# Kernel tuning notes

Hardware: AMD Instinct MI355X
Metric: run time of the kernel (lower is better)

Reference implementation:

```python
import jax, jax.numpy as jnp
import numpy as np

D_MODEL = 1024
H = 16
D_K = D_MODEL // H
D_FF = 4096
EPS = 1e-6
NEG = -1e9


def setup_inputs() -> dict:
    key = jax.random.key(0)
    ks = jax.random.split(key, 8)
    B, S = 2, 2048
    src = jax.random.normal(ks[0], (B, S, D_MODEL), dtype=jnp.float32)
    src_mask = jnp.ones((B, 1, 1, S), dtype=jnp.int32)
    sc = 1.0 / np.sqrt(D_MODEL)
    wq = jax.random.normal(ks[1], (D_MODEL, D_MODEL), jnp.float32) * sc
    wk = jax.random.normal(ks[2], (D_MODEL, D_MODEL), jnp.float32) * sc
    wv = jax.random.normal(ks[3], (D_MODEL, D_MODEL), jnp.float32) * sc
    wo = jax.random.normal(ks[4], (D_MODEL, D_MODEL), jnp.float32) * sc
    w1 = jax.random.normal(ks[5], (D_FF, D_MODEL), jnp.float32) * sc
    b1 = jnp.zeros((D_FF,), jnp.float32)
    w2 = jax.random.normal(ks[6], (D_MODEL, D_FF), jnp.float32) * (1.0 / np.sqrt(D_FF))
    b2 = jnp.zeros((D_MODEL,), jnp.float32)
    a1 = jnp.ones((1,), jnp.float32)
    be1 = jnp.zeros((1,), jnp.float32)
    a2 = jnp.ones((1,), jnp.float32)
    be2 = jnp.zeros((1,), jnp.float32)
    return dict(src=src, src_mask=src_mask, wq=wq, wk=wk, wv=wv, wo=wo,
                w1=w1, b1=b1, w2=w2, b2=b2, a1=a1, be1=be1, a2=a2, be2=be2)


def layer_norm(x, alpha, bias):
    # torch: mean + unbiased std (ddof=1), eps added to std
    mean = jnp.mean(x, axis=-1, keepdims=True)
    std = jnp.sqrt(jnp.var(x, axis=-1, keepdims=True, ddof=1))
    return alpha * (x - mean) / (std + EPS) + bias


def mha(x, mask, wq, wk, wv, wo):
    B, S, _ = x.shape
    def split(t):  # [B,S,D] -> [B,H,S,D_K]
        return t.reshape(B, S, H, D_K).transpose(0, 2, 1, 3)
    q = split(x @ wq.T)
    k = split(x @ wk.T)
    v = split(x @ wv.T)
    scores = jnp.einsum('bhqd,bhkd->bhqk', q, k) / np.sqrt(D_K)
    scores = jnp.where(mask == 0, NEG, scores)
    attn = jax.nn.softmax(scores, axis=-1)
    out = jnp.einsum('bhqk,bhkd->bhqd', attn, v)
    out = out.transpose(0, 2, 1, 3).reshape(B, S, D_MODEL)
    return out @ wo.T


def reference(src, src_mask, wq, wk, wv, wo, w1, b1, w2, b2, a1, be1, a2, be2):
    x = layer_norm(src, a1, be1)
    src = src + mha(x, src_mask, wq, wk, wv, wo)
    x = layer_norm(src, a2, be2)
    ff = jax.nn.relu(x @ w1.T + b1) @ w2.T + b2
    return src + ff
```

## Files before the change

kernel.cpp:

```cpp
#include <hip/hip_runtime.h>
#include <hip/hip_bf16.h>

typedef unsigned short u16;
typedef unsigned int u32;
typedef float floatx4 __attribute__((ext_vector_type(4)));
typedef __bf16 bf16x8 __attribute__((ext_vector_type(8)));
typedef u16 ushort4v __attribute__((ext_vector_type(4)));
typedef u16 ushort8v __attribute__((ext_vector_type(8)));

#define DEVI static __device__ __forceinline__

DEVI u16 f2bf(float f) {
    u32 u = __builtin_bit_cast(u32, f);
    u += 0x7fffu + ((u >> 16) & 1u);
    return (u16)(u >> 16);
}
DEVI float bf2f(u16 h) { return __builtin_bit_cast(float, (u32)h << 16); }

DEVI float fexp2(float x) { return __builtin_amdgcn_exp2f(x); }

DEVI u32 cvtpk_bf16(float lo, float hi) {
    u32 r;
    asm("v_cvt_pk_bf16_f32 %0, %1, %2" : "=v"(r) : "v"(lo), "v"(hi));
    return r;
}

DEVI void async_cp16(const u16* g, u16* l) {
    __builtin_amdgcn_global_load_lds((const __attribute__((address_space(1))) u32*)g,
                                     (__attribute__((address_space(3))) u32*)l, 16, 0, 0);
}

template<int N> DEVI void wait_vmcnt() {
    if constexpr (N == 0)      asm volatile("s_waitcnt vmcnt(0)" ::: "memory");
    else if constexpr (N == 2) asm volatile("s_waitcnt vmcnt(2)" ::: "memory");
    else if constexpr (N == 3) asm volatile("s_waitcnt vmcnt(3)" ::: "memory");
    else if constexpr (N == 4) asm volatile("s_waitcnt vmcnt(4)" ::: "memory");
    else if constexpr (N == 6) asm volatile("s_waitcnt vmcnt(6)" ::: "memory");
    else static_assert(N == 0, "add vmcnt case");
}

#define PH_BAR() asm volatile("s_barrier" ::: "memory")

template<bool QKV3, int NSPLIT, bool BIAS, bool RELU, bool VTW>
__global__ __launch_bounds__(512, 2) void gemm8p(
    const u16* __restrict__ A,
    const u16* __restrict__ W0, const u16* __restrict__ W1, const u16* __restrict__ W2,
    const float* __restrict__ bias,
    void* __restrict__ o0, void* __restrict__ o1, void* __restrict__ o2,
    void* __restrict__ o3, int K, int lda, int Nper, int NX)
{
    __shared__ __align__(16) u16 As[2][2][8192];
    __shared__ __align__(16) u16 Bs[2][2][8192];
    const int tid = threadIdx.x;
    const int w = tid >> 6, lane = tid & 63;
    const int q = lane >> 4, ml = lane & 15;
    const int wr = w >> 2, wc = w & 3;
    int bx = blockIdx.x, by = blockIdx.y;
    {
        const int gx = gridDim.x, gy = gridDim.y;
        int L = by * gx + bx;
        int xcd = L & 7, s = L >> 3;
        int mb = gy >> 3;
        by = xcd * mb + s % mb;
        bx = s / mb;
    }
    const int m0 = by * 256;
    size_t kbase = 0;
    const u16* W = W0;
    void* outp = o0;
    if (NSPLIT > 1) {
        int part = bx / NX; bx -= part * NX; kbase = (size_t)part * K;
        outp = (part == 0) ? o0 : (part == 1 ? o1 : (part == 2 ? o2 : o3));
    }
    int n0 = bx * 256;
    bool vwrite = false;
    if (QKV3) {
        int sel = n0 / Nper; n0 -= sel * Nper;
        W = (sel == 0) ? W0 : (sel == 1 ? W1 : W2);
        outp = (sel == 0) ? o0 : (sel == 1 ? o1 : o2);
        if (VTW) vwrite = (sel == 2);
    }

    auto stA = [&](int d, int kh, int kt) {
#pragma unroll
        for (int p = 0; p < 2; ++p) {
            int c = p * 512 + tid;
            int r = c >> 2;
            int sc = (c & 3) ^ ((r >> 1) & 3);
            async_cp16(A + (size_t)(m0 + r) * lda + kbase + kt + kh * 32 + sc * 8,
                       &As[d][kh][(p * 512 + w * 64) * 8]);
        }
    };
    auto stB = [&](int d, int kh, int kt) {
#pragma unroll
        for (int p = 0; p < 2; ++p) {
            int c = p * 512 + tid;
            int r = c >> 2;
            int sc = (c & 3) ^ ((r >> 1) & 3);
            async_cp16(W + (size_t)(n0 + r) * lda + kbase + kt + kh * 32 + sc * 8,
                       &Bs[d][kh][(p * 512 + w * 64) * 8]);
        }
    };
    auto rdA = [&](int d, int kh, int i) -> bf16x8 {
        int rm = wr * 128 + i * 16 + ml;
        return *(const bf16x8*)&As[d][kh][(rm * 4 + (q ^ ((rm >> 1) & 3))) * 8];
    };
    auto rdB = [&](int d, int kh, int j) -> bf16x8 {
        int rn = wc * 64 + j * 16 + ml;
        return *(const bf16x8*)&Bs[d][kh][(rn * 4 + (q ^ ((rn >> 1) & 3))) * 8];
    };

    const floatx4 fzero = {0.f, 0.f, 0.f, 0.f};
    floatx4 acc[8][4];
#pragma unroll
    for (int i = 0; i < 8; ++i)
#pragma unroll
        for (int j = 0; j < 4; ++j) acc[i][j] = fzero;

#define PHASE(d, kh, ih, STG, VM)                                              \
    {                                                                          \
        if (ih == 0) {                                                         \
            _Pragma("unroll")                                                  \
            for (int j = 0; j < 4; ++j) bfr[j] = rdB(d, kh, j);                \
        }                                                                      \
        _Pragma("unroll")                                                      \
        for (int ii = 0; ii < 4; ++ii) af[ii] = rdA(d, kh, (ih) * 4 + ii);     \
        STG;                                                                   \
        if (VM) wait_vmcnt<4>();                                               \
        PH_BAR();                                                              \
        __builtin_amdgcn_s_setprio(1);                                         \
        _Pragma("unroll")                                                      \
        for (int ii = 0; ii < 4; ++ii)                                         \
            _Pragma("unroll")                                                  \
            for (int j = 0; j < 4; ++j)                                        \
                acc[(ih) * 4 + ii][j] = __builtin_amdgcn_mfma_f32_16x16x32_bf16( \
                    af[ii], bfr[j], acc[(ih) * 4 + ii][j], 0, 0, 0);           \
        __builtin_amdgcn_s_setprio(0);                                         \
        PH_BAR();                                                              \
    }

    const int R = K >> 7;
    stA(0, 0, 0); stB(0, 0, 0); stA(0, 1, 0); stB(0, 1, 0);
    wait_vmcnt<0>();
    PH_BAR();

    for (int rr = 0; rr < R; ++rr) {
        const int kt1 = rr * 128 + 64;
        const int kt2 = (rr * 128 + 128 <= K - 64) ? rr * 128 + 128
                                                   : K - 64;
        bf16x8 af[4], bfr[4];
        PHASE(0, 0, 0, stA(1, 0, kt1), 0)
        PHASE(0, 0, 1, stB(1, 0, kt1), 1)
        PHASE(0, 1, 0, stA(1, 1, kt1), 0)
        PHASE(0, 1, 1, stB(1, 1, kt1), 1)
        PHASE(1, 0, 0, stA(0, 0, kt2), 0)
        PHASE(1, 0, 1, stB(0, 0, kt2), 1)
        PHASE(1, 1, 0, stA(0, 1, kt2), 0)
        PHASE(1, 1, 1, stB(0, 1, kt2), 1)
    }
#undef PHASE
    wait_vmcnt<0>();

#pragma unroll
    for (int j = 0; j < 4; ++j) {
        int gn = n0 + wc * 64 + j * 16 + ml;
        float bj = 0.f;
        if (BIAS) bj = bias[gn];
#pragma unroll
        for (int i = 0; i < 8; ++i) {
            int gm0 = m0 + wr * 128 + i * 16 + q * 4;
            if (VTW && vwrite) {
                int bb = gm0 >> 11, sres = gm0 & 2047;
                ushort4v o = {f2bf(acc[i][j][0]), f2bf(acc[i][j][1]),
                              f2bf(acc[i][j][2]), f2bf(acc[i][j][3])};
                *(ushort4v*)&((u16*)o3)[(size_t)(bb * 1024 + gn) * 2048 + sres] = o;
            } else {
#pragma unroll
                for (int r = 0; r < 4; ++r) {
                    size_t idx = (size_t)(gm0 + r) * Nper + gn;
                    float v = acc[i][j][r] + bj;
                    if (RELU) v = fmaxf(v, 0.f);
                    ((u16*)outp)[idx] = f2bf(v);
                }
            }
        }
    }
}

template<int BM, int BN, int RW, int CW, bool BIAS, bool RELU, bool RESID, bool OBF16>
__global__ __launch_bounds__(256) void gemm_nt(
    const u16* __restrict__ A, const u16* __restrict__ W0,
    const float* __restrict__ bias, const float* __restrict__ resid,
    void* __restrict__ o0, int K, int lda, int Nper)
{
    static_assert(RW * CW == 4, "4 waves");
    constexpr int WM = BM / RW, WN = BN / CW;
    constexpr int MI = WM / 16, NI = WN / 16;
    constexpr int LPT = BM / 64 + BN / 64;
    __shared__ __align__(16) u16 As[3][BM * 32];
    __shared__ __align__(16) u16 Bs[3][BN * 32];
    const int tid = threadIdx.x;
    const int w = tid >> 6, lane = tid & 63;
    const int q = lane >> 4, ml = lane & 15;
    const int wr = w / CW, wc = w % CW;
    int bx = blockIdx.x, by = blockIdx.y;
    {
        const int gx = gridDim.x, gy = gridDim.y;
        int L = by * gx + bx;
        int xcd = L & 7, s = L >> 3;
        int mb = gy >> 3;
        by = xcd * mb + s % mb;
        bx = s / mb;
    }
    const int m0 = by * BM;
    const u16* W = W0;
    int n0 = bx * BN;

    auto stage = [&](int buf, int kt) {
#pragma unroll
        for (int p = 0; p < BM / 64; ++p) {
            int g = p * 256 + tid;
            int r = g >> 2, s = g & 3;
            int c = s ^ ((r >> 1) & 3);
            async_cp16(A + (size_t)(m0 + r) * lda + kt + c * 8,
                       &As[buf][(p * 256 + w * 64) * 8]);
        }
#pragma unroll
        for (int p = 0; p < BN / 64; ++p) {
            int g = p * 256 + tid;
            int r = g >> 2, s = g & 3;
            int c = s ^ ((r >> 1) & 3);
            async_cp16(W + (size_t)(n0 + r) * lda + kt + c * 8,
                       &Bs[buf][(p * 256 + w * 64) * 8]);
        }
    };

    const floatx4 fzero = {0.f, 0.f, 0.f, 0.f};
    floatx4 acc[MI][NI];
#pragma unroll
    for (int i = 0; i < MI; ++i)
#pragma unroll
        for (int j = 0; j < NI; ++j) acc[i][j] = fzero;

    const int nt = K >> 5;
    stage(0, 0);
    stage(1, 32);
    int cb = 0, nb = 2;
    for (int it = 0, kt = 0; it < nt; ++it, kt += 32) {
        wait_vmcnt<LPT>();
        __builtin_amdgcn_s_barrier();
        __builtin_amdgcn_sched_barrier(0);
        if (it + 2 < nt) stage(nb, kt + 64);
        __builtin_amdgcn_sched_barrier(0);
        const u16* Asb = As[cb];
        const u16* Bsb = Bs[cb];
        bf16x8 af[MI], bfr[NI];
#pragma unroll
        for (int i = 0; i < MI; ++i) {
            int rm = wr * WM + i * 16 + ml;
            int s = q ^ ((rm >> 1) & 3);
            af[i] = *(const bf16x8*)&Asb[(rm * 4 + s) * 8];
        }
#pragma unroll
        for (int j = 0; j < NI; ++j) {
            int rn = wc * WN + j * 16 + ml;
            int s = q ^ ((rn >> 1) & 3);
            bfr[j] = *(const bf16x8*)&Bsb[(rn * 4 + s) * 8];
        }
#pragma unroll
        for (int i = 0; i < MI; ++i)
#pragma unroll
            for (int j = 0; j < NI; ++j)
                acc[i][j] = __builtin_amdgcn_mfma_f32_16x16x32_bf16(af[i], bfr[j], acc[i][j], 0, 0, 0);
        cb = cb == 2 ? 0 : cb + 1;
        nb = nb == 2 ? 0 : nb + 1;
    }

#pragma unroll
    for (int j = 0; j < NI; ++j) {
        int gn = n0 + wc * WN + j * 16 + ml;
        float bj = 0.f;
        if (BIAS) bj = bias[gn];
#pragma unroll
        for (int i = 0; i < MI; ++i) {
            int gm0 = m0 + wr * WM + i * 16 + q * 4;
#pragma unroll
            for (int r = 0; r < 4; ++r) {
                size_t idx = (size_t)(gm0 + r) * Nper + gn;
                float v = acc[i][j][r] + bj;
                if (RELU) v = fmaxf(v, 0.f);
                if (RESID) v += resid[idx];
                if (OBF16) ((u16*)o0)[idx] = f2bf(v);
                else       ((float*)o0)[idx] = v;
            }
        }
    }
}

__global__ __launch_bounds__(256, 2) void flash9(
    const u16* __restrict__ Q, const u16* __restrict__ Kg,
    const u16* __restrict__ Vt, const float* __restrict__ biasv,
    u16* __restrict__ O)
{
    __shared__ __align__(16) u16 smem[24576];
    const int tid = threadIdx.x;
    const int w = tid >> 6, lane = tid & 63;
    const int qw = w & 1, kv = w >> 1;
    const int q = lane >> 4, ml = lane & 15;
    const int b = blockIdx.y >> 4, h = blockIdx.y & 15;
    const size_t rowQ = (size_t)(b * 2048 + blockIdx.x * 128);
    const float KSC = 0.125f * 1.4426950408889634f;
    const floatx4 fzero = {0.f, 0.f, 0.f, 0.f};

    bf16x8 qa[4][2];
#pragma unroll
    for (int qg = 0; qg < 4; ++qg)
#pragma unroll
        for (int c = 0; c < 2; ++c)
            qa[qg][c] = *(const bf16x8*)&Q[(rowQ + qw * 64 + qg * 16 + ml) * 1024
                                           + h * 64 + q * 8 + c * 32];

    auto stage = [&](int buf, int it) {
        {
            int row = tid >> 3, sl = tid & 7;
            int ch = sl ^ ((row & 3) | (((row >> 3) & 1) << 2));
#pragma unroll
            for (int hf = 0; hf < 2; ++hf)
                async_cp16(Kg + (size_t)(b * 2048 + hf * 1024 + it * 32 + row) * 1024
                               + h * 64 + ch * 8,
                           &smem[(hf * 3 + buf) * 2048 + w * 512]);
        }
        {
            int row = tid >> 2, sl = tid & 3;
            int ch = sl ^ ((row >> 1) & 3);
#pragma unroll
            for (int hf = 0; hf < 2; ++hf)
                async_cp16(Vt + (size_t)(b * 1024 + h * 64 + row) * 2048
                               + hf * 1024 + it * 32 + ch * 8,
                           &smem[12288 + (hf * 3 + buf) * 2048 + w * 512]);
        }
    };

    floatx4 oacc[4][4];
    float lsum[4] = {0.f, 0.f, 0.f, 0.f};
#pragma unroll
    for (int qg = 0; qg < 4; ++qg)
#pragma unroll
        for (int d = 0; d < 4; ++d) oacc[qg][d] = fzero;

    const int swk = (ml & 3) | (((ml >> 2) & 1) << 2);
    const int re = ((ml >> 2) << 3) + (ml & 3);

    stage(0, 0);
    stage(1, 1);
    int cb = 0, nb = 2;
    for (int it = 0; it < 32; ++it) {
        asm volatile("s_waitcnt vmcnt(4)" ::: "memory");
        __builtin_amdgcn_s_barrier();
        __builtin_amdgcn_sched_barrier(0);
        const int s0 = kv * 1024 + it * 32;
        const float4 be = *(const float4*)&biasv[b * 2048 + s0 + q * 8];
        const float4 bo = *(const float4*)&biasv[b * 2048 + s0 + q * 8 + 4];
        __builtin_amdgcn_sched_barrier(0);
        stage(nb, it + 2 < 32 ? it + 2 : 31);

        const u16* Kb = &smem[(kv * 3 + cb) * 2048];
        const u16* Vb = &smem[12288 + (kv * 3 + cb) * 2048];

        bf16x8 ke0 = *(const bf16x8*)&Kb[(re + 0) * 64 + ((0 + q) ^ swk) * 8];
        bf16x8 ke1 = *(const bf16x8*)&Kb[(re + 0) * 64 + ((4 + q) ^ swk) * 8];
        bf16x8 ko0 = *(const bf16x8*)&Kb[(re + 4) * 64 + ((0 + q) ^ swk) * 8];
        bf16x8 ko1 = *(const bf16x8*)&Kb[(re + 4) * 64 + ((4 + q) ^ swk) * 8];
        bf16x8 pfrag[4];
#pragma unroll
        for (int qg = 0; qg < 4; ++qg) {
            floatx4 te = fzero, to = fzero;
            te = __builtin_amdgcn_mfma_f32_16x16x32_bf16(ke0, qa[qg][0], te, 0, 0, 0);
            te = __builtin_amdgcn_mfma_f32_16x16x32_bf16(ke1, qa[qg][1], te, 0, 0, 0);
            to = __builtin_amdgcn_mfma_f32_16x16x32_bf16(ko0, qa[qg][0], to, 0, 0, 0);
            to = __builtin_amdgcn_mfma_f32_16x16x32_bf16(ko1, qa[qg][1], to, 0, 0, 0);
            float pe0 = fexp2(fmaf(te[0], KSC, be.x));
            float pe1 = fexp2(fmaf(te[1], KSC, be.y));
            float pe2 = fexp2(fmaf(te[2], KSC, be.z));
            float pe3 = fexp2(fmaf(te[3], KSC, be.w));
            float po0 = fexp2(fmaf(to[0], KSC, bo.x));
            float po1 = fexp2(fmaf(to[1], KSC, bo.y));
            float po2 = fexp2(fmaf(to[2], KSC, bo.z));
            float po3 = fexp2(fmaf(to[3], KSC, bo.w));
            lsum[qg] += ((pe0 + pe1) + (pe2 + pe3)) + ((po0 + po1) + (po2 + po3));
            u32 pk[4];
            pk[0] = cvtpk_bf16(pe0, pe1);
            pk[1] = cvtpk_bf16(pe2, pe3);
            pk[2] = cvtpk_bf16(po0, po1);
            pk[3] = cvtpk_bf16(po2, po3);
            pfrag[qg] = __builtin_bit_cast(bf16x8, *(uint4*)pk);
        }
#pragma unroll
        for (int dt = 0; dt < 4; ++dt) {
            int vrow = dt * 16 + ml;
            bf16x8 vf = *(const bf16x8*)&Vb[vrow * 32 + ((q ^ ((vrow >> 1) & 3)) * 8)];
#pragma unroll
            for (int qg = 0; qg < 4; ++qg)
                oacc[qg][dt] = __builtin_amdgcn_mfma_f32_16x16x32_bf16(
                    vf, pfrag[qg], oacc[qg][dt], 0, 0, 0);
        }
        cb = cb == 2 ? 0 : cb + 1;
        nb = nb == 2 ? 0 : nb + 1;
    }

    __syncthreads();
    float* sO = (float*)smem;
    float* sL = (float*)smem + 8192;
    if (kv == 1) {
#pragma unroll
        for (int qg = 0; qg < 4; ++qg) {
            sL[(qw * 4 + qg) * 64 + lane] = lsum[qg];
#pragma unroll
            for (int dt = 0; dt < 4; ++dt)
                *(floatx4*)&sO[((qw * 4 + qg) * 4 + dt) * 256 + lane * 4] = oacc[qg][dt];
        }
    }
    __syncthreads();
    if (kv == 1) return;
#pragma unroll
    for (int qg = 0; qg < 4; ++qg) {
        lsum[qg] += sL[(qw * 4 + qg) * 64 + lane];
#pragma unroll
        for (int dt = 0; dt < 4; ++dt)
            oacc[qg][dt] += *(const floatx4*)&sO[((qw * 4 + qg) * 4 + dt) * 256 + lane * 4];
        float ls = lsum[qg];
        ls += __shfl_xor(ls, 16, 64);
        ls += __shfl_xor(ls, 32, 64);
        const float rcp = 1.f / ls;
        const size_t row = rowQ + qw * 64 + qg * 16 + ml;
#pragma unroll
        for (int dt = 0; dt < 4; ++dt)
#pragma unroll
            for (int rp = 0; rp < 4; rp += 2) {
                u32 pk = (u32)f2bf(oacc[qg][dt][rp] * rcp)
                       | ((u32)f2bf(oacc[qg][dt][rp + 1] * rcp) << 16);
                *(u32*)&O[row * 1024 + h * 64 + dt * 16 + q * 4 + rp] = pk;
            }
    }
}

DEVI void ln_row(const float* __restrict__ x, float ga, float gb,
                 u16* __restrict__ y, int row, int tid)
{
    const float4 v = ((const float4*)(x + (size_t)row * 1024))[tid];
    float s = v.x + v.y + v.z + v.w;
    float ss = v.x * v.x + v.y * v.y + v.z * v.z + v.w * v.w;
#pragma unroll
    for (int d = 1; d < 64; d <<= 1) { s += __shfl_xor(s, d, 64); ss += __shfl_xor(ss, d, 64); }
    __shared__ float ps[4], pss[4];
    const int w = tid >> 6, lane = tid & 63;
    if (lane == 0) { ps[w] = s; pss[w] = ss; }
    __syncthreads();
    s = ps[0] + ps[1] + ps[2] + ps[3];
    ss = pss[0] + pss[1] + pss[2] + pss[3];
    float mean = s * (1.f / 1024.f);
    float var = fmaxf((ss - s * mean) * (1.f / 1023.f), 0.f);
    float sc = ga / (sqrtf(var) + 1e-6f);
    ushort4v o;
    o[0] = f2bf((v.x - mean) * sc + gb);
    o[1] = f2bf((v.y - mean) * sc + gb);
    o[2] = f2bf((v.z - mean) * sc + gb);
    o[3] = f2bf((v.w - mean) * sc + gb);
    ((ushort4v*)(y + (size_t)row * 1024))[tid] = o;
}

__global__ __launch_bounds__(256) void ln_bf16(const float* __restrict__ x,
    const float* __restrict__ ga, const float* __restrict__ gb, u16* __restrict__ y)
{
    ln_row(x, ga[0], gb[0], y, blockIdx.x, threadIdx.x);
}

__global__ __launch_bounds__(256) void prep(
    const float* __restrict__ wq, const float* __restrict__ wk,
    const float* __restrict__ wv, const float* __restrict__ wo,
    const float* __restrict__ w1, const float* __restrict__ w2,
    u16* __restrict__ wqb, u16* __restrict__ wkb, u16* __restrict__ wvb,
    u16* __restrict__ wob, u16* __restrict__ w1b, u16* __restrict__ w2b,
    const int* __restrict__ m, float* __restrict__ biasv,
    const float* __restrict__ src, const float* __restrict__ a1,
    const float* __restrict__ be1, u16* __restrict__ xln1)
{
    const int bx = blockIdx.x;
    if (bx < 12288) {
        size_t i = (size_t)bx * 256 + threadIdx.x;
        const float* s; u16* d; size_t off;
        if (i < 262144)       { s = wq; d = wqb; off = i; }
        else if (i < 524288)  { s = wk; d = wkb; off = i - 262144; }
        else if (i < 786432)  { s = wv; d = wvb; off = i - 524288; }
        else if (i < 1048576) { s = wo; d = wob; off = i - 786432; }
        else if (i < 2097152) { s = w1; d = w1b; off = i - 1048576; }
        else                  { s = w2; d = w2b; off = i - 2097152; }
        float4 v = ((const float4*)s)[off];
        ushort4v o = {f2bf(v.x), f2bf(v.y), f2bf(v.z), f2bf(v.w)};
        ((ushort4v*)d)[off] = o;
    } else if (bx < 12304) {
        int i = (bx - 12288) * 256 + threadIdx.x;
        biasv[i] = m[i] ? 0.f : -1.442695e9f;
    } else {
        ln_row(src, a1[0], be1[0], xln1, bx - 12304, threadIdx.x);
    }
}

__global__ __launch_bounds__(256) void ff2_fin(
    const u16* __restrict__ p0, const u16* __restrict__ p1,
    const u16* __restrict__ p2, const u16* __restrict__ p3,
    const float* __restrict__ b2, const float* __restrict__ resid,
    float* __restrict__ out)
{
    const size_t i = (size_t)blockIdx.x * 256 + threadIdx.x;
    ushort4v a = *(const ushort4v*)&p0[i * 4];
    ushort4v b = *(const ushort4v*)&p1[i * 4];
    ushort4v c = *(const ushort4v*)&p2[i * 4];
    ushort4v d = *(const ushort4v*)&p3[i * 4];
    float4 r = ((const float4*)resid)[i];
    float4 bb = ((const float4*)b2)[i & 255];
    float4 o;
    o.x = ((bf2f(a[0]) + bf2f(b[0])) + (bf2f(c[0]) + bf2f(d[0]))) + r.x + bb.x;
    o.y = ((bf2f(a[1]) + bf2f(b[1])) + (bf2f(c[1]) + bf2f(d[1]))) + r.y + bb.y;
    o.z = ((bf2f(a[2]) + bf2f(b[2])) + (bf2f(c[2]) + bf2f(d[2]))) + r.z + bb.z;
    o.w = ((bf2f(a[3]) + bf2f(b[3])) + (bf2f(c[3]) + bf2f(d[3]))) + r.w + bb.w;
    ((float4*)out)[i] = o;
}

extern "C" void kernel_launch(void* const* d_in, const int* in_sizes, int n_in,
                              void* d_out, int out_size, void* d_ws, size_t ws_size,
                              hipStream_t stream)
{
    const float* src = (const float*)d_in[0];
    const int* msk   = (const int*)d_in[1];
    const float* wq  = (const float*)d_in[2];
    const float* wk  = (const float*)d_in[3];
    const float* wv  = (const float*)d_in[4];
    const float* wo  = (const float*)d_in[5];
    const float* w1  = (const float*)d_in[6];
    const float* b1  = (const float*)d_in[7];
    const float* w2  = (const float*)d_in[8];
    const float* b2  = (const float*)d_in[9];
    const float* a1  = (const float*)d_in[10];
    const float* be1 = (const float*)d_in[11];
    const float* a2  = (const float*)d_in[12];
    const float* be2 = (const float*)d_in[13];
    float* out = (float*)d_out;

    char* ws = (char*)d_ws;
    const size_t MB = (size_t)1 << 20;
    u16* wqb  = (u16*)(ws + 0 * MB);
    u16* wkb  = (u16*)(ws + 2 * MB);
    u16* wvb  = (u16*)(ws + 4 * MB);
    u16* wob  = (u16*)(ws + 6 * MB);
    u16* w1b  = (u16*)(ws + 8 * MB);
    u16* w2b  = (u16*)(ws + 16 * MB);
    u16* xln1 = (u16*)(ws + 24 * MB);
    u16* attn = xln1;
    u16* Qb   = (u16*)(ws + 32 * MB);
    u16* xln2 = Qb;
    u16* Kb   = (u16*)(ws + 40 * MB);
    u16* Vt   = (u16*)(ws + 56 * MB);
    float* biasv = (float*)(ws + 64 * MB);
    u16* h1   = (u16*)(ws + 40 * MB);
    float* src2 = (float*)(ws + 72 * MB);
    u16* P0 = (u16*)(ws + 0 * MB);
    u16* P1 = (u16*)(ws + 8 * MB);
    u16* P2 = (u16*)(ws + 24 * MB);
    u16* P3 = (u16*)(ws + 32 * MB);

    prep<<<16400, 256, 0, stream>>>(wq, wk, wv, wo, w1, w2,
                                    wqb, wkb, wvb, wob, w1b, w2b,
                                    msk, biasv, src, a1, be1, xln1);

    gemm8p<true, 1, false, false, true><<<dim3(12, 16), 512, 0, stream>>>(
        xln1, wqb, wkb, wvb, nullptr, Qb, Kb, nullptr, Vt, 1024, 1024, 1024, 0);

    flash9<<<dim3(16, 32), 256, 0, stream>>>(Qb, Kb, Vt, biasv, attn);

    gemm_nt<128, 64, 4, 1, false, false, true, false><<<dim3(16, 32), 256, 0, stream>>>(
        attn, wob, nullptr, src, src2, 1024, 1024, 1024);

    ln_bf16<<<4096, 256, 0, stream>>>(src2, a2, be2, xln2);

    gemm8p<false, 1, true, true, false><<<dim3(16, 16), 512, 0, stream>>>(
        xln2, w1b, nullptr, nullptr, b1, h1, nullptr, nullptr, nullptr,
        1024, 1024, 4096, 0);

    gemm8p<false, 4, false, false, false><<<dim3(16, 16), 512, 0, stream>>>(
        h1, w2b, nullptr, nullptr, nullptr, P0, P1, P2, P3,
        1024, 4096, 1024, 4);

    ff2_fin<<<4096, 256, 0, stream>>>(P0, P1, P2, P3, b2, src2, out);
}
```

Before: 348.2 us.

## Use generalized 256-thread gemm_nt for QKV projection and XCD-swizzle flash blocks

Generalizes gemm_nt to support QKV-fused output selection, split-K parts, and the transposed V write. The QKV projection now uses it with 128x128 tiles and 256-thread blocks instead of the 512-thread gemm8p, which gives a larger grid of smaller blocks. The attention kernel also remaps block indices so that blocks sharing the same batch and head land on the same XCD, aiming for better L2 reuse of K and V. In exchange, the QKV GEMM gives up gemm8p's deeper phased pipeline.

```diff
diff --git a/kernel.cpp b/kernel.cpp
--- a/kernel.cpp
+++ b/kernel.cpp
@@ -40,6 +40,140 @@
 }
 
 #define PH_BAR() asm volatile("s_barrier" ::: "memory")
+
+template<int BM, int BN, int RW, int CW, bool QKV3, int NSPLIT, bool XSWZ,
+         bool BIAS, bool RELU, bool RESID, bool OBF16, bool VTW>
+__global__ __launch_bounds__(256) void gemm_nt(
+    const u16* __restrict__ A,
+    const u16* __restrict__ W0, const u16* __restrict__ W1, const u16* __restrict__ W2,
+    const float* __restrict__ bias, const float* __restrict__ resid,
+    void* __restrict__ o0, void* __restrict__ o1, void* __restrict__ o2,
+    void* __restrict__ o3, int K, int lda, int Nper, int NX)
+{
+    static_assert(RW * CW == 4, "4 waves");
+    constexpr int WM = BM / RW, WN = BN / CW;
+    constexpr int MI = WM / 16, NI = WN / 16;
+    constexpr int LPT = BM / 64 + BN / 64;
+    __shared__ __align__(16) u16 As[3][BM * 32];
+    __shared__ __align__(16) u16 Bs[3][BN * 32];
+    const int tid = threadIdx.x;
+    const int w = tid >> 6, lane = tid & 63;
+    const int q = lane >> 4, ml = lane & 15;
+    const int wr = w / CW, wc = w % CW;
+    int bx = blockIdx.x, by = blockIdx.y;
+    if (XSWZ) {
+        const int gx = gridDim.x, gy = gridDim.y;
+        int L = by * gx + bx;
+        int xcd = L & 7, s = L >> 3;
+        int mb = gy >> 3;
+        by = xcd * mb + s % mb;
+        bx = s / mb;
+    }
+    const int m0 = by * BM;
+    size_t kbase = 0;
+    const u16* W = W0;
+    void* outp = o0;
+    if (NSPLIT > 1) {
+        int part = bx / NX; bx -= part * NX; kbase = (size_t)part * K;
+        outp = (part == 0) ? o0 : (part == 1 ? o1 : (part == 2 ? o2 : o3));
+    }
+    int n0 = bx * BN;
+    bool vwrite = false;
+    if (QKV3) {
+        int sel = n0 / Nper;
+        n0 -= sel * Nper;
+        W = (sel == 0) ? W0 : (sel == 1 ? W1 : W2);
+        outp = (sel == 0) ? o0 : (sel == 1 ? o1 : o2);
+        if (VTW) vwrite = (sel == 2);
+    }
+
+    auto stage = [&](int buf, int kt) {
+#pragma unroll
+        for (int p = 0; p < BM / 64; ++p) {
+            int g = p * 256 + tid;
+            int r = g >> 2, s = g & 3;
+            int c = s ^ ((r >> 1) & 3);
+            async_cp16(A + (size_t)(m0 + r) * lda + kbase + kt + c * 8,
+                       &As[buf][(p * 256 + w * 64) * 8]);
+        }
+#pragma unroll
+        for (int p = 0; p < BN / 64; ++p) {
+            int g = p * 256 + tid;
+            int r = g >> 2, s = g & 3;
+            int c = s ^ ((r >> 1) & 3);
+            async_cp16(W + (size_t)(n0 + r) * lda + kbase + kt + c * 8,
+                       &Bs[buf][(p * 256 + w * 64) * 8]);
+        }
+    };
+
+    const floatx4 fzero = {0.f, 0.f, 0.f, 0.f};
+    floatx4 acc[MI][NI];
+#pragma unroll
+    for (int i = 0; i < MI; ++i)
+#pragma unroll
+        for (int j = 0; j < NI; ++j) acc[i][j] = fzero;
+
+    const int nt = K >> 5;
+    stage(0, 0);
+    stage(1, 32);
+    int cb = 0, nb = 2;
+    for (int it = 0, kt = 0; it < nt; ++it, kt += 32) {
+        wait_vmcnt<LPT>();
+        __builtin_amdgcn_s_barrier();
+        __builtin_amdgcn_sched_barrier(0);
+        if (it + 2 < nt) stage(nb, kt + 64);
+        __builtin_amdgcn_sched_barrier(0);
+        const u16* Asb = As[cb];
+        const u16* Bsb = Bs[cb];
+        bf16x8 af[MI], bfr[NI];
+#pragma unroll
+        for (int i = 0; i < MI; ++i) {
+            int rm = wr * WM + i * 16 + ml;
+            int s = q ^ ((rm >> 1) & 3);
+            af[i] = *(const bf16x8*)&Asb[(rm * 4 + s) * 8];
+        }
+#pragma unroll
+        for (int j = 0; j < NI; ++j) {
+            int rn = wc * WN + j * 16 + ml;
+            int s = q ^ ((rn >> 1) & 3);
+            bfr[j] = *(const bf16x8*)&Bsb[(rn * 4 + s) * 8];
+        }
+#pragma unroll
+        for (int i = 0; i < MI; ++i)
+#pragma unroll
+            for (int j = 0; j < NI; ++j)
+                acc[i][j] = __builtin_amdgcn_mfma_f32_16x16x32_bf16(af[i], bfr[j], acc[i][j], 0, 0, 0);
+        cb = cb == 2 ? 0 : cb + 1;
+        nb = nb == 2 ? 0 : nb + 1;
+    }
+
+#pragma unroll
+    for (int j = 0; j < NI; ++j) {
+        int gn = n0 + wc * WN + j * 16 + ml;
+        float bj = 0.f;
+        if (BIAS) bj = bias[gn];
+#pragma unroll
+        for (int i = 0; i < MI; ++i) {
+            int gm0 = m0 + wr * WM + i * 16 + q * 4;
+            if (VTW && vwrite) {
+                int bb = gm0 >> 11, sres = gm0 & 2047;
+                ushort4v o = {f2bf(acc[i][j][0]), f2bf(acc[i][j][1]),
+                              f2bf(acc[i][j][2]), f2bf(acc[i][j][3])};
+                *(ushort4v*)&((u16*)o3)[(size_t)(bb * 1024 + gn) * 2048 + sres] = o;
+            } else {
+#pragma unroll
+                for (int r = 0; r < 4; ++r) {
+                    size_t idx = (size_t)(gm0 + r) * Nper + gn;
+                    float v = acc[i][j][r] + bj;
+                    if (RELU) v = fmaxf(v, 0.f);
+                    if (RESID) v += resid[idx];
+                    if (OBF16) ((u16*)outp)[idx] = f2bf(v);
+                    else       ((float*)outp)[idx] = v;
+                }
+            }
+        }
+    }
+}
 
 template<bool QKV3, int NSPLIT, bool BIAS, bool RELU, bool VTW>
 __global__ __launch_bounds__(512, 2) void gemm8p(
@@ -146,8 +280,7 @@
 
     for (int rr = 0; rr < R; ++rr) {
         const int kt1 = rr * 128 + 64;
-        const int kt2 = (rr * 128 + 128 <= K - 64) ? rr * 128 + 128
-                                                   : K - 64;
+        const int kt2 = (rr * 128 + 128 <= K - 64) ? rr * 128 + 128 : K - 64;
         bf16x8 af[4], bfr[4];
         PHASE(0, 0, 0, stA(1, 0, kt1), 0)
         PHASE(0, 0, 1, stB(1, 0, kt1), 1)
@@ -187,116 +320,6 @@
     }
 }
 
-template<int BM, int BN, int RW, int CW, bool BIAS, bool RELU, bool RESID, bool OBF16>
-__global__ __launch_bounds__(256) void gemm_nt(
-    const u16* __restrict__ A, const u16* __restrict__ W0,
-    const float* __restrict__ bias, const float* __restrict__ resid,
-    void* __restrict__ o0, int K, int lda, int Nper)
-{
-    static_assert(RW * CW == 4, "4 waves");
-    constexpr int WM = BM / RW, WN = BN / CW;
-    constexpr int MI = WM / 16, NI = WN / 16;
-    constexpr int LPT = BM / 64 + BN / 64;
-    __shared__ __align__(16) u16 As[3][BM * 32];
-    __shared__ __align__(16) u16 Bs[3][BN * 32];
-    const int tid = threadIdx.x;
-    const int w = tid >> 6, lane = tid & 63;
-    const int q = lane >> 4, ml = lane & 15;
-    const int wr = w / CW, wc = w % CW;
-    int bx = blockIdx.x, by = blockIdx.y;
-    {
-        const int gx = gridDim.x, gy = gridDim.y;
-        int L = by * gx + bx;
-        int xcd = L & 7, s = L >> 3;
-        int mb = gy >> 3;
-        by = xcd * mb + s % mb;
-        bx = s / mb;
-    }
-    const int m0 = by * BM;
-    const u16* W = W0;
-    int n0 = bx * BN;
-
-    auto stage = [&](int buf, int kt) {
-#pragma unroll
-        for (int p = 0; p < BM / 64; ++p) {
-            int g = p * 256 + tid;
-            int r = g >> 2, s = g & 3;
-            int c = s ^ ((r >> 1) & 3);
-            async_cp16(A + (size_t)(m0 + r) * lda + kt + c * 8,
-                       &As[buf][(p * 256 + w * 64) * 8]);
-        }
-#pragma unroll
-        for (int p = 0; p < BN / 64; ++p) {
-            int g = p * 256 + tid;
-            int r = g >> 2, s = g & 3;
-            int c = s ^ ((r >> 1) & 3);
-            async_cp16(W + (size_t)(n0 + r) * lda + kt + c * 8,
-                       &Bs[buf][(p * 256 + w * 64) * 8]);
-        }
-    };
-
-    const floatx4 fzero = {0.f, 0.f, 0.f, 0.f};
-    floatx4 acc[MI][NI];
-#pragma unroll
-    for (int i = 0; i < MI; ++i)
-#pragma unroll
-        for (int j = 0; j < NI; ++j) acc[i][j] = fzero;
-
-    const int nt = K >> 5;
-    stage(0, 0);
-    stage(1, 32);
-    int cb = 0, nb = 2;
-    for (int it = 0, kt = 0; it < nt; ++it, kt += 32) {
-        wait_vmcnt<LPT>();
-        __builtin_amdgcn_s_barrier();
-        __builtin_amdgcn_sched_barrier(0);
-        if (it + 2 < nt) stage(nb, kt + 64);
-        __builtin_amdgcn_sched_barrier(0);
-        const u16* Asb = As[cb];
-        const u16* Bsb = Bs[cb];
-        bf16x8 af[MI], bfr[NI];
-#pragma unroll
-        for (int i = 0; i < MI; ++i) {
-            int rm = wr * WM + i * 16 + ml;
-            int s = q ^ ((rm >> 1) & 3);
-            af[i] = *(const bf16x8*)&Asb[(rm * 4 + s) * 8];
-        }
-#pragma unroll
-        for (int j = 0; j < NI; ++j) {
-            int rn = wc * WN + j * 16 + ml;
-            int s = q ^ ((rn >> 1) & 3);
-            bfr[j] = *(const bf16x8*)&Bsb[(rn * 4 + s) * 8];
-        }
-#pragma unroll
-        for (int i = 0; i < MI; ++i)
-#pragma unroll
-            for (int j = 0; j < NI; ++j)
-                acc[i][j] = __builtin_amdgcn_mfma_f32_16x16x32_bf16(af[i], bfr[j], acc[i][j], 0, 0, 0);
-        cb = cb == 2 ? 0 : cb + 1;
-        nb = nb == 2 ? 0 : nb + 1;
-    }
-
-#pragma unroll
-    for (int j = 0; j < NI; ++j) {
-        int gn = n0 + wc * WN + j * 16 + ml;
-        float bj = 0.f;
-        if (BIAS) bj = bias[gn];
-#pragma unroll
-        for (int i = 0; i < MI; ++i) {
-            int gm0 = m0 + wr * WM + i * 16 + q * 4;
-#pragma unroll
-            for (int r = 0; r < 4; ++r) {
-                size_t idx = (size_t)(gm0 + r) * Nper + gn;
-                float v = acc[i][j][r] + bj;
-                if (RELU) v = fmaxf(v, 0.f);
-                if (RESID) v += resid[idx];
-                if (OBF16) ((u16*)o0)[idx] = f2bf(v);
-                else       ((float*)o0)[idx] = v;
-            }
-        }
-    }
-}
-
 __global__ __launch_bounds__(256, 2) void flash9(
     const u16* __restrict__ Q, const u16* __restrict__ Kg,
     const u16* __restrict__ Vt, const float* __restrict__ biasv,
@@ -307,8 +330,15 @@
     const int w = tid >> 6, lane = tid & 63;
     const int qw = w & 1, kv = w >> 1;
     const int q = lane >> 4, ml = lane & 15;
-    const int b = blockIdx.y >> 4, h = blockIdx.y & 15;
-    const size_t rowQ = (size_t)(b * 2048 + blockIdx.x * 128);
+    int bx = blockIdx.x, by = blockIdx.y;
+    {
+        int L = by * 16 + bx;
+        int xcd = L & 7, s = L >> 3;
+        by = xcd * 4 + (s >> 4);
+        bx = s & 15;
+    }
+    const int b = by >> 4, h = by & 15;
+    const size_t rowQ = (size_t)(b * 2048 + bx * 128);
     const float KSC = 0.125f * 1.4426950408889634f;
     const floatx4 fzero = {0.f, 0.f, 0.f, 0.f};
 
@@ -573,13 +603,14 @@
                                     wqb, wkb, wvb, wob, w1b, w2b,
                                     msk, biasv, src, a1, be1, xln1);
 
-    gemm8p<true, 1, false, false, true><<<dim3(12, 16), 512, 0, stream>>>(
-        xln1, wqb, wkb, wvb, nullptr, Qb, Kb, nullptr, Vt, 1024, 1024, 1024, 0);
+    gemm_nt<128, 128, 2, 2, true, 1, true, false, false, false, true, true><<<dim3(24, 32), 256, 0, stream>>>(
+        xln1, wqb, wkb, wvb, nullptr, nullptr, Qb, Kb, nullptr, Vt, 1024, 1024, 1024, 0);
 
     flash9<<<dim3(16, 32), 256, 0, stream>>>(Qb, Kb, Vt, biasv, attn);
 
-    gemm_nt<128, 64, 4, 1, false, false, true, false><<<dim3(16, 32), 256, 0, stream>>>(
-        attn, wob, nullptr, src, src2, 1024, 1024, 1024);
+    gemm_nt<128, 64, 4, 1, false, 1, true, false, false, true, false, false><<<dim3(16, 32), 256, 0, stream>>>(
+        attn, wob, nullptr, nullptr, nullptr, src, src2, nullptr, nullptr, nullptr,
+        1024, 1024, 1024, 0);
 
     ln_bf16<<<4096, 256, 0, stream>>>(src2, a2, be2, xln2);
 
```

Measured after the change: 322.4 us. 7.4% less time.
